# Optimization experiments

Hardware: AMD Instinct MI355X
Metric: run time of the kernel (lower is better)

Reference implementation:

```python
import jax, jax.numpy as jnp
import numpy as np

B, S, D = 4, 2048, 1024
E, H, K = 32, 128, 2


def setup_inputs() -> dict:
    key = jax.random.key(0)
    k1, k2, k3, k4 = jax.random.split(key, 4)
    scale_d = 1.0 / np.sqrt(D)
    scale_h = 1.0 / np.sqrt(H)
    return {
        "x": jax.random.normal(k1, (B, S, D), dtype=jnp.float32),
        "w_sel": jax.random.normal(k2, (E, D), dtype=jnp.float32) * scale_d,      # router Linear weight [E, D]
        "w_keys": jax.random.normal(k3, (E, D, H), dtype=jnp.float32) * scale_d,  # per-expert up-proj
        "w_values": jax.random.normal(k4, (E, H, D), dtype=jnp.float32) * scale_h, # per-expert down-proj
        "k": K,
    }


def reference(x, w_sel, w_keys, w_values, k):
    # Router: sigmoid gating + top-k expert selection per token.
    sel = jax.nn.sigmoid(jnp.einsum('bsd,ed->bse', x, w_sel))      # [B,S,E]
    sel_val, sel_idx = jax.lax.top_k(sel, k)                       # [B,S,k]
    n_exp = w_sel.shape[0]
    # Dense gate matrix: gate[b,s,e] = sum of sel_val over heads routed to e
    # (top_k indices are distinct, so this matches the per-head accumulation).
    gate = jnp.sum(jax.nn.one_hot(sel_idx, n_exp, dtype=x.dtype) * sel_val[..., None], axis=-2)  # [B,S,E]
    # Expert up-projection + ReLU for all experts (dense equivalent of the
    # per-token gathered keys[expert_idx](token); unselected experts are
    # zeroed by the gate so the math is identical).
    scores = jax.nn.relu(jnp.einsum('bsd,edh->bseh', x, w_keys))   # [B,S,E,H]
    weighted = scores * gate[..., None]                            # [B,S,E,H]
    out = jnp.einsum('bseh,ehd->bsd', weighted, w_values)          # [B,S,D]
    return out
```

## Files before the change

### kernel.cpp

```cpp
#include <hip/hip_runtime.h>
#include <cstdint>
#include <cstddef>

#define NTOK 8192
#define DIM  1024
#define NEXP 32
#define NH   128
#define TT   16
#define NSLOT 64
#define BK   128
#define RT   32
#define LCAP 1024
#define NRB  (NTOK / RT)
#define NTRB 2048
#define NCVB 512

typedef __attribute__((ext_vector_type(8))) short short8;
typedef __attribute__((ext_vector_type(4))) float float4_;

static __device__ __forceinline__ unsigned short f2bf(float f) {
  unsigned u = __float_as_uint(f);
  return (unsigned short)((u + 0x7fffu + ((u >> 16) & 1u)) >> 16);
}
static __device__ __forceinline__ float bf2f(unsigned short h) {
  return __uint_as_float(((unsigned)h) << 16);
}
static __device__ __forceinline__ void gload_lds16(const unsigned short* g,
                                                   unsigned short* l) {
  __builtin_amdgcn_global_load_lds(
      (const __attribute__((address_space(1))) unsigned int*)(const void*)g,
      (__attribute__((address_space(3))) unsigned int*)(void*)l, 16, 0, 0);
}

__global__ __launch_bounds__(256) void prep_router_kernel(
    const float* __restrict__ x, const float* __restrict__ w_sel,
    const float* __restrict__ w_keys, const float* __restrict__ w_values,
    unsigned short* __restrict__ xbf, unsigned short* __restrict__ wk_t,
    unsigned short* __restrict__ wv_t,
    int* __restrict__ counts, unsigned* __restrict__ list)
{
  __shared__ __align__(16) char smem[22656];
  const int bid = blockIdx.x;
  const int tid = threadIdx.x;

  if (bid >= NRB + NTRB) {
    const int lb = bid - NRB - NTRB;
    #pragma unroll
    for (int q = 0; q < 4; ++q) {
      const size_t off = (size_t)lb * 16384 + (size_t)q * 4096 + (size_t)tid * 16;
      float4 v0 = *(const float4*)(x + off);
      float4 v1 = *(const float4*)(x + off + 4);
      float4 v2 = *(const float4*)(x + off + 8);
      float4 v3 = *(const float4*)(x + off + 12);
      uint4 u0, u1;
      u0.x = (unsigned)f2bf(v0.x) | ((unsigned)f2bf(v0.y) << 16);
      u0.y = (unsigned)f2bf(v0.z) | ((unsigned)f2bf(v0.w) << 16);
      u0.z = (unsigned)f2bf(v1.x) | ((unsigned)f2bf(v1.y) << 16);
      u0.w = (unsigned)f2bf(v1.z) | ((unsigned)f2bf(v1.w) << 16);
      u1.x = (unsigned)f2bf(v2.x) | ((unsigned)f2bf(v2.y) << 16);
      u1.y = (unsigned)f2bf(v2.z) | ((unsigned)f2bf(v2.w) << 16);
      u1.z = (unsigned)f2bf(v3.x) | ((unsigned)f2bf(v3.y) << 16);
      u1.w = (unsigned)f2bf(v3.z) | ((unsigned)f2bf(v3.w) << 16);
      *(uint4*)(xbf + off)     = u0;
      *(uint4*)(xbf + off + 8) = u1;
    }
    return;
  }

  if (bid >= NRB) {
    float (*tile)[65] = (float (*)[65])smem;
    const int lb = bid - NRB;
    const float* src; unsigned short* dst; int R, C, e, t, tpc;
    if (lb < 1024) { src = w_keys;   dst = wk_t; R = DIM; C = NH;  e = lb >> 5;          t = lb & 31; tpc = 2; }
    else           { src = w_values; dst = wv_t; R = NH;  C = DIM; e = (lb - 1024) >> 5; t = (lb - 1024) & 31; tpc = 16; }
    const int r0 = (t / tpc) * 64;
    const int c0 = (t % tpc) * 64;
    const float* s = src + (size_t)e * R * C;
    unsigned short* d = dst + (size_t)e * R * C;

    const int i  = tid >> 2;
    const int j0 = (tid & 3) * 16;
    #pragma unroll
    for (int k4 = 0; k4 < 4; ++k4) {
      float4 v = *(const float4*)(s + (size_t)(r0 + i) * C + c0 + j0 + k4 * 4);
      tile[i][j0 + k4 * 4 + 0] = v.x;
      tile[i][j0 + k4 * 4 + 1] = v.y;
      tile[i][j0 + k4 * 4 + 2] = v.z;
      tile[i][j0 + k4 * 4 + 3] = v.w;
    }
    __syncthreads();
    unsigned pk[8];
    #pragma unroll
    for (int k = 0; k < 8; ++k) {
      unsigned lo = f2bf(tile[j0 + 2 * k][i]);
      unsigned hi = f2bf(tile[j0 + 2 * k + 1][i]);
      pk[k] = lo | (hi << 16);
    }
    uint4 u0; u0.x = pk[0]; u0.y = pk[1]; u0.z = pk[2]; u0.w = pk[3];
    uint4 u1; u1.x = pk[4]; u1.y = pk[5]; u1.z = pk[6]; u1.w = pk[7];
    unsigned short* dp = d + (size_t)(c0 + i) * R + r0 + j0;
    *(uint4*)(dp)     = u0;
    *(uint4*)(dp + 8) = u1;
    return;
  }

  float (*xs_t)[36] = (float (*)[36])smem;
  float (*ws_t)[36] = (float (*)[36])(smem + 9216);
  float (*S)[33]    = (float (*)[33])(smem + 18432);
  float (*red)[64][16] = (float (*)[64][16])smem;

  const int tok0 = bid * RT;
  const int wv   = tid >> 6;
  const int lane = tid & 63;
  const int tr   = tid >> 3;
  const int i8   = tid & 7;
  const int d8   = i8 * 8;
  const int swzW = i8 << 2;
  const int tg4  = (lane & 7) * 4;
  const int eg4  = (lane >> 3) * 4;
  const int dlo  = wv * 16;

  float acc[16];
  #pragma unroll
  for (int k = 0; k < 16; ++k) acc[k] = 0.f;

  float4 a0, a1, b0, b1;
  {
    const float* xp = x + (size_t)(tok0 + tr) * DIM + d8;
    a0 = *(const float4*)(xp);
    a1 = *(const float4*)(xp + 4);
    const float* wp = w_sel + (size_t)tr * DIM + d8;
    b0 = *(const float4*)(wp);
    b1 = *(const float4*)(wp + 4);
  }

  for (int c = 0; c < 16; ++c) {
    const int dc = c * 64;

    {
      const int colx = tr ^ swzW;
      xs_t[d8 + 0][colx] = a0.x; xs_t[d8 + 1][colx] = a0.y;
      xs_t[d8 + 2][colx] = a0.z; xs_t[d8 + 3][colx] = a0.w;
      xs_t[d8 + 4][colx] = a1.x; xs_t[d8 + 5][colx] = a1.y;
      xs_t[d8 + 6][colx] = a1.z; xs_t[d8 + 7][colx] = a1.w;
      ws_t[d8 + 0][colx] = b0.x; ws_t[d8 + 1][colx] = b0.y;
      ws_t[d8 + 2][colx] = b0.z; ws_t[d8 + 3][colx] = b0.w;
      ws_t[d8 + 4][colx] = b1.x; ws_t[d8 + 5][colx] = b1.y;
      ws_t[d8 + 6][colx] = b1.z; ws_t[d8 + 7][colx] = b1.w;
    }
    __syncthreads();

    if (c < 15) {
      const float* xp = x + (size_t)(tok0 + tr) * DIM + dc + 64 + d8;
      a0 = *(const float4*)(xp);
      a1 = *(const float4*)(xp + 4);
      const float* wp = w_sel + (size_t)tr * DIM + dc + 64 + d8;
      b0 = *(const float4*)(wp);
      b1 = *(const float4*)(wp + 4);
    }

    #pragma unroll
    for (int dd = 0; dd < 16; ++dd) {
      const int d  = dlo + dd;
      const int sz = (d >> 3) << 2;
      float4 xv = *(const float4*)&xs_t[d][tg4 ^ sz];
      float4 w4 = *(const float4*)&ws_t[d][eg4 ^ sz];
      acc[0]  = fmaf(w4.x, xv.x, acc[0]);  acc[1]  = fmaf(w4.x, xv.y, acc[1]);
      acc[2]  = fmaf(w4.x, xv.z, acc[2]);  acc[3]  = fmaf(w4.x, xv.w, acc[3]);
      acc[4]  = fmaf(w4.y, xv.x, acc[4]);  acc[5]  = fmaf(w4.y, xv.y, acc[5]);
      acc[6]  = fmaf(w4.y, xv.z, acc[6]);  acc[7]  = fmaf(w4.y, xv.w, acc[7]);
      acc[8]  = fmaf(w4.z, xv.x, acc[8]);  acc[9]  = fmaf(w4.z, xv.y, acc[9]);
      acc[10] = fmaf(w4.z, xv.z, acc[10]); acc[11] = fmaf(w4.z, xv.w, acc[11]);
      acc[12] = fmaf(w4.w, xv.x, acc[12]); acc[13] = fmaf(w4.w, xv.y, acc[13]);
      acc[14] = fmaf(w4.w, xv.z, acc[14]); acc[15] = fmaf(w4.w, xv.w, acc[15]);
    }
    __syncthreads();
  }

  #pragma unroll
  for (int ei = 0; ei < 4; ++ei) {
    float4 v; v.x = acc[ei * 4 + 0]; v.y = acc[ei * 4 + 1];
    v.z = acc[ei * 4 + 2]; v.w = acc[ei * 4 + 3];
    *(float4*)&red[wv][lane][ei * 4] = v;
  }
  __syncthreads();

  {
    const int eg2 = tid >> 5, tg2 = (tid >> 2) & 7, ei2 = tid & 3;
    const int cls = eg2 * 8 + tg2;
    float4 s4; s4.x = 0.f; s4.y = 0.f; s4.z = 0.f; s4.w = 0.f;
    #pragma unroll
    for (int w = 0; w < 4; ++w) {
      float4 v = *(const float4*)&red[w][cls][ei2 * 4];
      s4.x += v.x; s4.y += v.y; s4.z += v.z; s4.w += v.w;
    }
    S[tg2 * 4 + 0][eg2 * 4 + ei2] = s4.x;
    S[tg2 * 4 + 1][eg2 * 4 + ei2] = s4.y;
    S[tg2 * 4 + 2][eg2 * 4 + ei2] = s4.z;
    S[tg2 * 4 + 3][eg2 * 4 + ei2] = s4.w;
  }
  __syncthreads();

  if (tid < RT) {
    const int t = tid;
    float m1 = -1e30f, m2 = -1e30f;
    int i1 = 0, i2 = 0;
    for (int ee = 0; ee < NEXP; ++ee) {
      float v = S[t][ee];
      if (v > m1)      { m2 = m1; i2 = i1; m1 = v; i1 = ee; }
      else if (v > m2) { m2 = v; i2 = ee; }
    }
    const int token = tok0 + t;
    float g1 = 1.f / (1.f + __expf(-m1));
    float g2 = 1.f / (1.f + __expf(-m2));
    unsigned e1 = ((unsigned)f2bf(g1) << 16) | ((unsigned)token << 1);
    unsigned e2 = ((unsigned)f2bf(g2) << 16) | ((unsigned)token << 1) | 1u;
    int p1 = atomicAdd(&counts[i1], 1);
    if (p1 < LCAP) list[i1 * LCAP + p1] = e1;
    int p2 = atomicAdd(&counts[i2], 1);
    if (p2 < LCAP) list[i2 * LCAP + p2] = e2;
  }
}

__global__ __launch_bounds__(256, 4) void ffn_kernel(
    const unsigned short* __restrict__ xbf,
    const unsigned short* __restrict__ wk_t,
    const unsigned short* __restrict__ wv_t,
    float* __restrict__ out,
    unsigned short* __restrict__ cont,
    const int* __restrict__ counts, const unsigned* __restrict__ list,
    int use_cont)
{
  const int bid = blockIdx.x;
  const int e   = bid & 31;
  const int cnt = min(counts[e], LCAP);
  const int t0  = (bid >> 5) * TT;
  if (t0 >= cnt) return;

  __shared__ __align__(16) unsigned short uni[4224];
  __shared__ unsigned short ss[TT][NH + 8];
  __shared__ int   toks[TT];
  __shared__ float gates[TT];
  unsigned short (*xsf)[2048] = (unsigned short (*)[2048])uni;
  unsigned short (*st)[264]   = (unsigned short (*)[264])uni;

  const int tid  = threadIdx.x;
  const int wave = tid >> 6;
  const int lane = tid & 63;
  const int quad = lane >> 4;
  const int l16  = lane & 15;

  const unsigned short* wkb = wk_t + (size_t)e * NH * DIM;
  const unsigned short* wvb = wv_t + (size_t)e * DIM * NH;
  const int n_tok = min(TT, cnt - t0);

  if (tid < TT) {
    int valid = tid < n_tok;
    unsigned en = valid ? list[e * LCAP + t0 + tid] : 0u;
    toks[tid]  = valid ? (int)(en & 0xffffu) : -1;
    gates[tid] = valid ? bf2f((unsigned short)(en >> 16)) : 0.f;
  }
  __syncthreads();

  {
    int sl   = toks[l16];
    int gtok = (sl < 0) ? 0 : (sl >> 1);
    const unsigned short* gsrc = xbf + (size_t)gtok * DIM + quad * 8;

    gload_lds16(gsrc + wave * 32, &xsf[0][wave * 512]);
    __syncthreads();

    float4_ acc[2];
    acc[0] = (float4_){0.f, 0.f, 0.f, 0.f};
    acc[1] = (float4_){0.f, 0.f, 0.f, 0.f};

    for (int ci = 0; ci < 8; ++ci) {
      const int dc = ci * BK;
      if (ci < 7)
        gload_lds16(gsrc + dc + BK + wave * 32, &xsf[(ci + 1) & 1][wave * 512]);

      short8 b[4][2];
      #pragma unroll
      for (int kk = 0; kk < 4; ++kk)
        #pragma unroll
        for (int nt = 0; nt < 2; ++nt)
          b[kk][nt] = *(const short8*)(wkb +
              (size_t)(wave * 32 + nt * 16 + l16) * DIM + dc + kk * 32 + quad * 8);

      const unsigned short* xb = &xsf[ci & 1][0];
      #pragma unroll
      for (int kk = 0; kk < 4; ++kk) {
        short8 a = *(const short8*)(xb + kk * 512 + lane * 8);
        acc[0] = __builtin_amdgcn_mfma_f32_16x16x32_bf16(a, b[kk][0], acc[0], 0, 0, 0);
        acc[1] = __builtin_amdgcn_mfma_f32_16x16x32_bf16(a, b[kk][1], acc[1], 0, 0, 0);
      }
      __syncthreads();
    }

    #pragma unroll
    for (int nt = 0; nt < 2; ++nt)
      #pragma unroll
      for (int r = 0; r < 4; ++r) {
        int row = quad * 4 + r;
        float v = fmaxf(acc[nt][r], 0.f) * gates[row];
        ss[row][wave * 32 + nt * 16 + l16] = f2bf(v);
      }
  }
  __syncthreads();

  #pragma unroll 1
  for (int nc = 0; nc < 4; ++nc) {
    const int colbase = wave * 256 + nc * 64;
    float4_ o[4];
    #pragma unroll
    for (int nt = 0; nt < 4; ++nt) o[nt] = (float4_){0.f, 0.f, 0.f, 0.f};

    #pragma unroll
    for (int kk = 0; kk < 4; ++kk) {
      short8 bk[4];
      #pragma unroll
      for (int nt = 0; nt < 4; ++nt)
        bk[nt] = *(const short8*)(wvb +
            (size_t)(colbase + nt * 16 + l16) * NH + kk * 32 + quad * 8);
      short8 a0 = *(const short8*)&ss[l16][kk * 32 + quad * 8];
      #pragma unroll
      for (int nt = 0; nt < 4; ++nt)
        o[nt] = __builtin_amdgcn_mfma_f32_16x16x32_bf16(a0, bk[nt], o[nt], 0, 0, 0);
    }

    if (use_cont) {
      #pragma unroll
      for (int nt = 0; nt < 4; ++nt)
        #pragma unroll
        for (int r = 0; r < 4; ++r)
          st[quad * 4 + r][wave * 64 + nt * 16 + l16] = f2bf(o[nt][r]);
      __syncthreads();
      #pragma unroll
      for (int q = 0; q < 2; ++q) {
        int idx = q * 256 + tid;
        int row = idx >> 5, seg = idx & 31;
        if (row < n_tok) {
          int sl2 = toks[row];
          size_t base = ((size_t)((sl2 & 1) * NTOK + (sl2 >> 1))) * DIM
                        + (seg >> 3) * 256 + nc * 64 + (seg & 7) * 8;
          *(short8*)&cont[base] = *(const short8*)&st[row][seg * 8];
        }
      }
      __syncthreads();
    } else {
      #pragma unroll
      for (int r = 0; r < 4; ++r) {
        int row = quad * 4 + r;
        if (row < n_tok) {
          size_t base = (size_t)(toks[row] >> 1) * DIM + colbase;
          #pragma unroll
          for (int nt = 0; nt < 4; ++nt)
            unsafeAtomicAdd(&out[base + nt * 16 + l16], o[nt][r]);
        }
      }
    }
  }
}

__global__ __launch_bounds__(256) void combine_kernel(
    const unsigned short* __restrict__ cont, float* __restrict__ out)
{
  size_t i = ((size_t)blockIdx.x * 256 + threadIdx.x) * 8;
  uint4 a = *(const uint4*)(cont + i);
  uint4 b = *(const uint4*)(cont + (size_t)NTOK * DIM + i);
  float4 r0, r1;
  r0.x = bf2f((unsigned short)(a.x & 0xffff)) + bf2f((unsigned short)(b.x & 0xffff));
  r0.y = bf2f((unsigned short)(a.x >> 16))    + bf2f((unsigned short)(b.x >> 16));
  r0.z = bf2f((unsigned short)(a.y & 0xffff)) + bf2f((unsigned short)(b.y & 0xffff));
  r0.w = bf2f((unsigned short)(a.y >> 16))    + bf2f((unsigned short)(b.y >> 16));
  r1.x = bf2f((unsigned short)(a.z & 0xffff)) + bf2f((unsigned short)(b.z & 0xffff));
  r1.y = bf2f((unsigned short)(a.z >> 16))    + bf2f((unsigned short)(b.z >> 16));
  r1.z = bf2f((unsigned short)(a.w & 0xffff)) + bf2f((unsigned short)(b.w & 0xffff));
  r1.w = bf2f((unsigned short)(a.w >> 16))    + bf2f((unsigned short)(b.w >> 16));
  *(float4*)(out + i) = r0;
  *(float4*)(out + i + 4) = r1;
}

extern "C" void kernel_launch(void* const* d_in, const int* in_sizes, int n_in,
                              void* d_out, int out_size, void* d_ws, size_t ws_size,
                              hipStream_t stream) {
  (void)in_sizes; (void)n_in;
  const float* x        = (const float*)d_in[0];
  const float* w_sel    = (const float*)d_in[1];
  const float* w_keys   = (const float*)d_in[2];
  const float* w_values = (const float*)d_in[3];
  float* out = (float*)d_out;

  char* ws = (char*)d_ws;
  size_t off = 0;
  int*            counts = (int*)(ws + off);            off += 4096;
  unsigned*       list   = (unsigned*)(ws + off);       off += (size_t)NEXP * LCAP * 4;
  unsigned short* wk_t   = (unsigned short*)(ws + off); off += (size_t)NEXP * NH * DIM * 2;
  unsigned short* wv_t   = (unsigned short*)(ws + off); off += (size_t)NEXP * NH * DIM * 2;
  unsigned short* xbf    = (unsigned short*)(ws + off); off += (size_t)NTOK * DIM * 2;
  unsigned short* cont   = (unsigned short*)(ws + off);
  size_t need_full = off + (size_t)2 * NTOK * DIM * 2;
  const int use_cont = (ws_size >= need_full) ? 1 : 0;

  hipMemsetAsync(counts, 0, NEXP * sizeof(int), stream);

  prep_router_kernel<<<NRB + NTRB + NCVB, 256, 0, stream>>>(
      x, w_sel, w_keys, w_values, xbf, wk_t, wv_t, counts, list);

  if (!use_cont)
    hipMemsetAsync(out, 0, (size_t)out_size * sizeof(float), stream);

  ffn_kernel<<<NEXP * NSLOT, 256, 0, stream>>>(xbf, wk_t, wv_t, out, cont,
                                               counts, list, use_cont);

  if (use_cont)
    combine_kernel<<<NTOK * DIM / (256 * 8), 256, 0, stream>>>(cont, out);
}
```

Baseline: 242.7 us.

## Double token tile to 32 and load x directly into registers

Raises the per-block token tile from 16 to 32 so each expert-weight fragment loaded from global memory feeds two MFMA row tiles, halving weight traffic per token in both the up- and down-projection. The LDS double-buffered async staging of x (global_load_lds plus per-chunk barriers) is replaced by direct global loads into registers, removing the syncs inside the K loop. In exchange the block count halves, register and LDS use per block grow, and partially filled tiles waste more work for experts with few tokens.

```diff
diff --git a/kernel.cpp b/kernel.cpp
--- a/kernel.cpp
+++ b/kernel.cpp
@@ -6,8 +6,8 @@
 #define DIM  1024
 #define NEXP 32
 #define NH   128
-#define TT   16
-#define NSLOT 64
+#define TT   32
+#define NSLOT 32
 #define BK   128
 #define RT   32
 #define LCAP 1024
@@ -24,12 +24,6 @@
 }
 static __device__ __forceinline__ float bf2f(unsigned short h) {
   return __uint_as_float(((unsigned)h) << 16);
-}
-static __device__ __forceinline__ void gload_lds16(const unsigned short* g,
-                                                   unsigned short* l) {
-  __builtin_amdgcn_global_load_lds(
-      (const __attribute__((address_space(1))) unsigned int*)(const void*)g,
-      (__attribute__((address_space(3))) unsigned int*)(void*)l, 16, 0, 0);
 }
 
 __global__ __launch_bounds__(256) void prep_router_kernel(
@@ -237,12 +231,10 @@
   const int t0  = (bid >> 5) * TT;
   if (t0 >= cnt) return;
 
-  __shared__ __align__(16) unsigned short uni[4224];
   __shared__ unsigned short ss[TT][NH + 8];
+  __shared__ unsigned short st[TT][264];
   __shared__ int   toks[TT];
   __shared__ float gates[TT];
-  unsigned short (*xsf)[2048] = (unsigned short (*)[2048])uni;
-  unsigned short (*st)[264]   = (unsigned short (*)[264])uni;
 
   const int tid  = threadIdx.x;
   const int wave = tid >> 6;
@@ -263,57 +255,57 @@
   __syncthreads();
 
   {
-    int sl   = toks[l16];
-    int gtok = (sl < 0) ? 0 : (sl >> 1);
-    const unsigned short* gsrc = xbf + (size_t)gtok * DIM + quad * 8;
-
-    gload_lds16(gsrc + wave * 32, &xsf[0][wave * 512]);
-    __syncthreads();
-
-    float4_ acc[2];
-    acc[0] = (float4_){0.f, 0.f, 0.f, 0.f};
-    acc[1] = (float4_){0.f, 0.f, 0.f, 0.f};
-
+    int sl0 = toks[l16];        int g0 = (sl0 < 0) ? 0 : (sl0 >> 1);
+    int sl1 = toks[16 + l16];   int g1 = (sl1 < 0) ? 0 : (sl1 >> 1);
+    const unsigned short* a0p = xbf + (size_t)g0 * DIM + quad * 8;
+    const unsigned short* a1p = xbf + (size_t)g1 * DIM + quad * 8;
+    const unsigned short* b0p = wkb + (size_t)(wave * 32 + l16) * DIM + quad * 8;
+    const unsigned short* b1p = wkb + (size_t)(wave * 32 + 16 + l16) * DIM + quad * 8;
+
+    float4_ acc[2][2];
+    #pragma unroll
+    for (int mt = 0; mt < 2; ++mt)
+      #pragma unroll
+      for (int nt = 0; nt < 2; ++nt) acc[mt][nt] = (float4_){0.f, 0.f, 0.f, 0.f};
+
+    #pragma unroll 2
     for (int ci = 0; ci < 8; ++ci) {
       const int dc = ci * BK;
-      if (ci < 7)
-        gload_lds16(gsrc + dc + BK + wave * 32, &xsf[(ci + 1) & 1][wave * 512]);
-
-      short8 b[4][2];
-      #pragma unroll
-      for (int kk = 0; kk < 4; ++kk)
+      #pragma unroll
+      for (int kk = 0; kk < 4; ++kk) {
+        const int d = dc + kk * 32;
+        short8 a0 = *(const short8*)(a0p + d);
+        short8 a1 = *(const short8*)(a1p + d);
+        short8 b0 = *(const short8*)(b0p + d);
+        short8 b1 = *(const short8*)(b1p + d);
+        acc[0][0] = __builtin_amdgcn_mfma_f32_16x16x32_bf16(a0, b0, acc[0][0], 0, 0, 0);
+        acc[0][1] = __builtin_amdgcn_mfma_f32_16x16x32_bf16(a0, b1, acc[0][1], 0, 0, 0);
+        acc[1][0] = __builtin_amdgcn_mfma_f32_16x16x32_bf16(a1, b0, acc[1][0], 0, 0, 0);
+        acc[1][1] = __builtin_amdgcn_mfma_f32_16x16x32_bf16(a1, b1, acc[1][1], 0, 0, 0);
+      }
+    }
+
+    #pragma unroll
+    for (int mt = 0; mt < 2; ++mt)
+      #pragma unroll
+      for (int nt = 0; nt < 2; ++nt)
         #pragma unroll
-        for (int nt = 0; nt < 2; ++nt)
-          b[kk][nt] = *(const short8*)(wkb +
-              (size_t)(wave * 32 + nt * 16 + l16) * DIM + dc + kk * 32 + quad * 8);
-
-      const unsigned short* xb = &xsf[ci & 1][0];
-      #pragma unroll
-      for (int kk = 0; kk < 4; ++kk) {
-        short8 a = *(const short8*)(xb + kk * 512 + lane * 8);
-        acc[0] = __builtin_amdgcn_mfma_f32_16x16x32_bf16(a, b[kk][0], acc[0], 0, 0, 0);
-        acc[1] = __builtin_amdgcn_mfma_f32_16x16x32_bf16(a, b[kk][1], acc[1], 0, 0, 0);
-      }
-      __syncthreads();
-    }
-
-    #pragma unroll
-    for (int nt = 0; nt < 2; ++nt)
-      #pragma unroll
-      for (int r = 0; r < 4; ++r) {
-        int row = quad * 4 + r;
-        float v = fmaxf(acc[nt][r], 0.f) * gates[row];
-        ss[row][wave * 32 + nt * 16 + l16] = f2bf(v);
-      }
+        for (int r = 0; r < 4; ++r) {
+          int row = mt * 16 + quad * 4 + r;
+          float v = fmaxf(acc[mt][nt][r], 0.f) * gates[row];
+          ss[row][wave * 32 + nt * 16 + l16] = f2bf(v);
+        }
   }
   __syncthreads();
 
   #pragma unroll 1
   for (int nc = 0; nc < 4; ++nc) {
     const int colbase = wave * 256 + nc * 64;
-    float4_ o[4];
-    #pragma unroll
-    for (int nt = 0; nt < 4; ++nt) o[nt] = (float4_){0.f, 0.f, 0.f, 0.f};
+    float4_ o[2][4];
+    #pragma unroll
+    for (int mt = 0; mt < 2; ++mt)
+      #pragma unroll
+      for (int nt = 0; nt < 4; ++nt) o[mt][nt] = (float4_){0.f, 0.f, 0.f, 0.f};
 
     #pragma unroll
     for (int kk = 0; kk < 4; ++kk) {
@@ -323,20 +315,25 @@
         bk[nt] = *(const short8*)(wvb +
             (size_t)(colbase + nt * 16 + l16) * NH + kk * 32 + quad * 8);
       short8 a0 = *(const short8*)&ss[l16][kk * 32 + quad * 8];
-      #pragma unroll
-      for (int nt = 0; nt < 4; ++nt)
-        o[nt] = __builtin_amdgcn_mfma_f32_16x16x32_bf16(a0, bk[nt], o[nt], 0, 0, 0);
+      short8 a1 = *(const short8*)&ss[16 + l16][kk * 32 + quad * 8];
+      #pragma unroll
+      for (int nt = 0; nt < 4; ++nt) {
+        o[0][nt] = __builtin_amdgcn_mfma_f32_16x16x32_bf16(a0, bk[nt], o[0][nt], 0, 0, 0);
+        o[1][nt] = __builtin_amdgcn_mfma_f32_16x16x32_bf16(a1, bk[nt], o[1][nt], 0, 0, 0);
+      }
     }
 
     if (use_cont) {
       #pragma unroll
-      for (int nt = 0; nt < 4; ++nt)
+      for (int mt = 0; mt < 2; ++mt)
         #pragma unroll
-        for (int r = 0; r < 4; ++r)
-          st[quad * 4 + r][wave * 64 + nt * 16 + l16] = f2bf(o[nt][r]);
+        for (int nt = 0; nt < 4; ++nt)
+          #pragma unroll
+          for (int r = 0; r < 4; ++r)
+            st[mt * 16 + quad * 4 + r][wave * 64 + nt * 16 + l16] = f2bf(o[mt][nt][r]);
       __syncthreads();
       #pragma unroll
-      for (int q = 0; q < 2; ++q) {
+      for (int q = 0; q < 4; ++q) {
         int idx = q * 256 + tid;
         int row = idx >> 5, seg = idx & 31;
         if (row < n_tok) {
@@ -349,15 +346,17 @@
       __syncthreads();
     } else {
       #pragma unroll
-      for (int r = 0; r < 4; ++r) {
-        int row = quad * 4 + r;
-        if (row < n_tok) {
-          size_t base = (size_t)(toks[row] >> 1) * DIM + colbase;
-          #pragma unroll
-          for (int nt = 0; nt < 4; ++nt)
-            unsafeAtomicAdd(&out[base + nt * 16 + l16], o[nt][r]);
+      for (int mt = 0; mt < 2; ++mt)
+        #pragma unroll
+        for (int r = 0; r < 4; ++r) {
+          int row = mt * 16 + quad * 4 + r;
+          if (row < n_tok) {
+            size_t base = (size_t)(toks[row] >> 1) * DIM + colbase;
+            #pragma unroll
+            for (int nt = 0; nt < 4; ++nt)
+              unsafeAtomicAdd(&out[base + nt * 16 + l16], o[mt][nt][r]);
+          }
         }
-      }
     }
   }
 }
```

New measurement: 230.0 us. 5.2% less time.
